# Optimization experiments

Hardware: AMD Instinct MI355X
Metric: run time of the kernel (lower is better)

The kernel has to match this reference:

```python
import jax, jax.numpy as jnp
import numpy as np

N_NODES = 100000
N_EDGES = 1600000

def spmm(edge_src, edge_dst, edge_w, h):
    # sparse adj (COO) @ dense h: gather source rows, scale, scatter-add to dest
    msg = h[edge_src] * edge_w[:, None]          # [E, F]
    return jax.ops.segment_sum(msg, edge_dst, num_segments=N_NODES)


def setup_inputs() -> dict:
    key = jax.random.key(0)
    ks = jax.random.split(key, 10)
    x = jax.random.normal(ks[0], (N_NODES, 128), dtype=jnp.float32)
    edge_src = jax.random.randint(ks[1], (N_EDGES,), 0, N_NODES, dtype=jnp.int32)
    edge_dst = jax.random.randint(ks[2], (N_EDGES,), 0, N_NODES, dtype=jnp.int32)
    edge_w = jax.random.uniform(ks[3], (N_EDGES,), dtype=jnp.float32)
    W1 = jax.random.normal(ks[4], (128, 64), dtype=jnp.float32) * 0.1
    b1 = jax.random.normal(ks[5], (64,), dtype=jnp.float32) * 0.1
    W2 = jax.random.normal(ks[6], (64, 64), dtype=jnp.float32) * 0.1
    b2 = jax.random.normal(ks[7], (64,), dtype=jnp.float32) * 0.1
    Wl = jax.random.normal(ks[8], (64, 40), dtype=jnp.float32) * 0.1
    bl = jax.random.normal(ks[9], (40,), dtype=jnp.float32) * 0.1
    return {"x": x, "edge_src": edge_src, "edge_dst": edge_dst, "edge_w": edge_w,
            "W1": W1, "b1": b1, "W2": W2, "b2": b2, "Wl": Wl, "bl": bl}


def reference(x, edge_src, edge_dst, edge_w, W1, b1, W2, b2, Wl, bl):
    # layer 1: relu(spmm(adj, x @ W1) + b1); dropout is identity in eval mode
    h1 = jax.nn.relu(spmm(edge_src, edge_dst, edge_w, x @ W1) + b1)
    # layer 2
    h2 = jax.nn.relu(spmm(edge_src, edge_dst, edge_w, h1 @ W2) + b2)
    # classifier head
    logits = h2 @ Wl + bl
    logp = jax.nn.log_softmax(logits, axis=1)
    # matches torch return: (log_softmax, node_emb=[h1, h2, logits])
    return (logp, h1, h2, logits)
```

## Files before the change

kernel.cpp:

```cpp
#include <hip/hip_runtime.h>
#include <hip/hip_bf16.h>
#include <math.h>

#define NN 100000
#define NE 1600000
#define BSHIFT 9
#define NBUCK ((NN + (1 << BSHIFT) - 1) >> BSHIFT)
#define CAP 10240
#define BINB 512
#define BCHUNK 1536
#define BINGRID ((NE + BCHUNK - 1) / BCHUNK)
#define HROWS 128
#define NPW 8

typedef __attribute__((ext_vector_type(8))) short bf16x8;
typedef __attribute__((ext_vector_type(4))) float f32x4;

static __device__ inline unsigned short f2b(float f) {
    __hip_bfloat16 b = __float2bfloat16(f);
    return *reinterpret_cast<unsigned short*>(&b);
}

__global__ __launch_bounds__(256) void gemm1_mfma(const float* __restrict__ x,
                                                  const float* __restrict__ W,
                                                  __hip_bfloat16* __restrict__ out) {
    __shared__ unsigned short Xs[128 * 136];
    __shared__ unsigned short Wt[64 * 136];
    const int tid = threadIdx.x;
    const int row0 = blockIdx.x * 128;
    for (int i = tid; i < 64 * 64; i += 256) {
        const int n = i & 63, kp = i >> 6;
        const unsigned pack = (unsigned)f2b(W[(2 * kp) * 64 + n]) |
                              ((unsigned)f2b(W[(2 * kp + 1) * 64 + n]) << 16);
        *(unsigned*)&Wt[n * 136 + 2 * kp] = pack;
    }
    for (int i = tid; i < 128 * 16; i += 256) {
        const int r = i >> 4, q = i & 15;
        const int row = row0 + r;
        float v0 = 0.f, v1 = 0.f, v2 = 0.f, v3 = 0.f, v4 = 0.f, v5 = 0.f, v6 = 0.f, v7 = 0.f;
        if (row < NN) {
            const float4 a = *(const float4*)(x + (size_t)row * 128 + q * 8);
            const float4 b = *(const float4*)(x + (size_t)row * 128 + q * 8 + 4);
            v0 = a.x; v1 = a.y; v2 = a.z; v3 = a.w; v4 = b.x; v5 = b.y; v6 = b.z; v7 = b.w;
        }
        uint4 pk;
        pk.x = (unsigned)f2b(v0) | ((unsigned)f2b(v1) << 16);
        pk.y = (unsigned)f2b(v2) | ((unsigned)f2b(v3) << 16);
        pk.z = (unsigned)f2b(v4) | ((unsigned)f2b(v5) << 16);
        pk.w = (unsigned)f2b(v6) | ((unsigned)f2b(v7) << 16);
        *(uint4*)&Xs[r * 136 + q * 8] = pk;
    }
    __syncthreads();
    const int l = tid & 63;
    const int wid = tid >> 6;
    const int m = l & 15, g = l >> 4;
    const int wr0 = wid * 32;
    f32x4 acc[2][4];
#pragma unroll
    for (int rt = 0; rt < 2; ++rt)
#pragma unroll
        for (int ct = 0; ct < 4; ++ct) acc[rt][ct] = 0;
#pragma unroll
    for (int ks = 0; ks < 4; ++ks) {
        bf16x8 a[2], b[4];
#pragma unroll
        for (int rt = 0; rt < 2; ++rt)
            a[rt] = *(const bf16x8*)&Xs[(wr0 + rt * 16 + m) * 136 + ks * 32 + g * 8];
#pragma unroll
        for (int ct = 0; ct < 4; ++ct)
            b[ct] = *(const bf16x8*)&Wt[(ct * 16 + m) * 136 + ks * 32 + g * 8];
#pragma unroll
        for (int rt = 0; rt < 2; ++rt)
#pragma unroll
            for (int ct = 0; ct < 4; ++ct)
                acc[rt][ct] = __builtin_amdgcn_mfma_f32_16x16x32_bf16(a[rt], b[ct], acc[rt][ct], 0, 0, 0);
    }
#pragma unroll
    for (int rt = 0; rt < 2; ++rt)
#pragma unroll
        for (int ct = 0; ct < 4; ++ct)
#pragma unroll
            for (int j = 0; j < 4; ++j) {
                const int r = row0 + wr0 + rt * 16 + g * 4 + j;
                if (r < NN)
                    out[(size_t)r * 64 + ct * 16 + m] = __float2bfloat16(acc[rt][ct][j]);
            }
}

__global__ __launch_bounds__(256) void gemm2_mfma(const float* __restrict__ h,
                                                  const float* __restrict__ W,
                                                  __hip_bfloat16* __restrict__ out) {
    __shared__ unsigned short Xs[128 * 72];
    __shared__ unsigned short Wt[64 * 72];
    const int tid = threadIdx.x;
    const int row0 = blockIdx.x * 128;
    for (int i = tid; i < 64 * 32; i += 256) {
        const int n = i & 63, kp = i >> 6;
        const unsigned pack = (unsigned)f2b(W[(2 * kp) * 64 + n]) |
                              ((unsigned)f2b(W[(2 * kp + 1) * 64 + n]) << 16);
        *(unsigned*)&Wt[n * 72 + 2 * kp] = pack;
    }
    for (int i = tid; i < 128 * 8; i += 256) {
        const int r = i >> 3, q = i & 7;
        const int row = row0 + r;
        float v0 = 0.f, v1 = 0.f, v2 = 0.f, v3 = 0.f, v4 = 0.f, v5 = 0.f, v6 = 0.f, v7 = 0.f;
        if (row < NN) {
            const float4 a = *(const float4*)(h + (size_t)row * 64 + q * 8);
            const float4 b = *(const float4*)(h + (size_t)row * 64 + q * 8 + 4);
            v0 = a.x; v1 = a.y; v2 = a.z; v3 = a.w; v4 = b.x; v5 = b.y; v6 = b.z; v7 = b.w;
        }
        uint4 pk;
        pk.x = (unsigned)f2b(v0) | ((unsigned)f2b(v1) << 16);
        pk.y = (unsigned)f2b(v2) | ((unsigned)f2b(v3) << 16);
        pk.z = (unsigned)f2b(v4) | ((unsigned)f2b(v5) << 16);
        pk.w = (unsigned)f2b(v6) | ((unsigned)f2b(v7) << 16);
        *(uint4*)&Xs[r * 72 + q * 8] = pk;
    }
    __syncthreads();
    const int l = tid & 63;
    const int wid = tid >> 6;
    const int m = l & 15, g = l >> 4;
    const int wr0 = wid * 32;
    f32x4 acc[2][4];
#pragma unroll
    for (int rt = 0; rt < 2; ++rt)
#pragma unroll
        for (int ct = 0; ct < 4; ++ct) acc[rt][ct] = 0;
#pragma unroll
    for (int ks = 0; ks < 2; ++ks) {
        bf16x8 a[2], b[4];
#pragma unroll
        for (int rt = 0; rt < 2; ++rt)
            a[rt] = *(const bf16x8*)&Xs[(wr0 + rt * 16 + m) * 72 + ks * 32 + g * 8];
#pragma unroll
        for (int ct = 0; ct < 4; ++ct)
            b[ct] = *(const bf16x8*)&Wt[(ct * 16 + m) * 72 + ks * 32 + g * 8];
#pragma unroll
        for (int rt = 0; rt < 2; ++rt)
#pragma unroll
            for (int ct = 0; ct < 4; ++ct)
                acc[rt][ct] = __builtin_amdgcn_mfma_f32_16x16x32_bf16(a[rt], b[ct], acc[rt][ct], 0, 0, 0);
    }
#pragma unroll
    for (int rt = 0; rt < 2; ++rt)
#pragma unroll
        for (int ct = 0; ct < 4; ++ct)
#pragma unroll
            for (int j = 0; j < 4; ++j) {
                const int r = row0 + wr0 + rt * 16 + g * 4 + j;
                if (r < NN)
                    out[(size_t)r * 64 + ct * 16 + m] = __float2bfloat16(acc[rt][ct][j]);
            }
}

__global__ void init_bcur(int* __restrict__ bcur) {
    const int t = threadIdx.x;
    if (t < NBUCK) bcur[t] = t * CAP;
}

__global__ __launch_bounds__(BINB) void bin_edges(const int* __restrict__ es,
                                                  const int* __restrict__ ed,
                                                  const float* __restrict__ ew,
                                                  int* __restrict__ bcur,
                                                  int2* __restrict__ srcdw) {
    __shared__ int hist[NBUCK];
    __shared__ int base[NBUCK];
    const int tid = threadIdx.x;
    const int e0 = blockIdx.x * BCHUNK;
    for (int i = tid; i < NBUCK; i += BINB) hist[i] = 0;
    __syncthreads();
    int d[3];
#pragma unroll
    for (int j = 0; j < 3; ++j) {
        const int e = e0 + j * BINB + tid;
        d[j] = (e < NE) ? ed[e] : -1;
        if (d[j] >= 0) atomicAdd(&hist[d[j] >> BSHIFT], 1);
    }
    __syncthreads();
    for (int i = tid; i < NBUCK; i += BINB) base[i] = atomicAdd(&bcur[i], hist[i]);
    __syncthreads();
    for (int i = tid; i < NBUCK; i += BINB) hist[i] = 0;
    __syncthreads();
#pragma unroll
    for (int j = 0; j < 3; ++j) {
        const int e = e0 + j * BINB + tid;
        if (d[j] >= 0) {
            const int bb = d[j] >> BSHIFT;
            const int l = atomicAdd(&hist[bb], 1);
            srcdw[base[bb] + l] = make_int2(es[e] | ((d[j] & 511) << 17), __float_as_int(ew[e]));
        }
    }
}

__global__ __launch_bounds__(1024) void bucket_csr(const int2* __restrict__ srcdw,
                                                   const int* __restrict__ bcur,
                                                   int2* __restrict__ rng,
                                                   int2* __restrict__ edges2) {
    __shared__ int A[512], B2[512];
    const int tid = threadIdx.x;
    const int b = blockIdx.x;
    const int base = b * CAP;
    const int cnt = bcur[b] - base;
    if (tid < 512) A[tid] = 0;
    __syncthreads();
    for (int e = tid; e < cnt; e += 1024)
        atomicAdd(&A[(srcdw[base + e].x >> 17) & 511], 1);
    __syncthreads();
    const int v = (tid < 512) ? A[tid] : 0;
    int* src = A;
    int* dst = B2;
    for (int d = 1; d < 512; d <<= 1) {
        if (tid < 512) dst[tid] = src[tid] + ((tid >= d) ? src[tid - d] : 0);
        __syncthreads();
        int* t = src; src = dst; dst = t;
    }
    if (tid < 512) {
        const int incl = src[tid];
        const int excl = incl - v;
        const int node = (b << BSHIFT) + tid;
        if (node < NN) rng[node] = make_int2(base + excl, base + incl);
        dst[tid] = excl;
    }
    __syncthreads();
    for (int e = tid; e < cnt; e += 1024) {
        const int2 sw = srcdw[base + e];
        const int dl = (sw.x >> 17) & 511;
        const int pos = atomicAdd(&dst[dl], 1);
        edges2[base + pos] = make_int2(sw.x & 0x1FFFF, sw.y);
    }
}

__global__ __launch_bounds__(256) void spmm_csr(const __hip_bfloat16* __restrict__ feat,
                                                const int2* __restrict__ rng,
                                                const int2* __restrict__ edges2,
                                                const float* __restrict__ b,
                                                float* __restrict__ out) {
    const int nwg = gridDim.x;
    const int q = nwg >> 3, rr = nwg & 7;
    const int xcd = blockIdx.x & 7;
    const int sub = blockIdx.x >> 3;
    const int swz = (xcd < rr ? xcd * (q + 1) : rr * (q + 1) + (xcd - rr) * q) + sub;
    const int w = threadIdx.x >> 6;
    const int lane = threadIdx.x & 63;
    const int n0 = (swz * 4 + w) * NPW;
    const int p = lane >> 3;
    const int f8 = lane & 7;
    const float4 bv0 = *(const float4*)(b + f8 * 8);
    const float4 bv1 = *(const float4*)(b + f8 * 8 + 4);
    const int2 r8 = rng[n0 + f8];
#define FMA8(G, WV)                                            \
    a0 = fmaf(__uint_as_float((G).x << 16), (WV), a0);         \
    a1 = fmaf(__uint_as_float((G).x & 0xffff0000u), (WV), a1); \
    a2 = fmaf(__uint_as_float((G).y << 16), (WV), a2);         \
    a3 = fmaf(__uint_as_float((G).y & 0xffff0000u), (WV), a3); \
    a4 = fmaf(__uint_as_float((G).z << 16), (WV), a4);         \
    a5 = fmaf(__uint_as_float((G).z & 0xffff0000u), (WV), a5); \
    a6 = fmaf(__uint_as_float((G).w << 16), (WV), a6);         \
    a7 = fmaf(__uint_as_float((G).w & 0xffff0000u), (WV), a7);
#define RED(A) A += __shfl_xor(A, 8, 64); A += __shfl_xor(A, 16, 64); A += __shfl_xor(A, 32, 64);
#pragma unroll 1
    for (int nn = 0; nn < NPW; ++nn) {
        const int n = n0 + nn;
        const int beg = __shfl(r8.x, nn, 64);
        const int end = __shfl(r8.y, nn, 64);
        float a0 = 0.f, a1 = 0.f, a2 = 0.f, a3 = 0.f;
        float a4 = 0.f, a5 = 0.f, a6 = 0.f, a7 = 0.f;
        int i = beg;
        for (; i + 15 < end; i += 16) {
            const int2 e0 = edges2[i + p];
            const int2 e1 = edges2[i + 8 + p];
            const uint4 g0 = *(const uint4*)(feat + (size_t)e0.x * 64 + f8 * 8);
            const uint4 g1 = *(const uint4*)(feat + (size_t)e1.x * 64 + f8 * 8);
            const float w0 = __int_as_float(e0.y), w1 = __int_as_float(e1.y);
            FMA8(g0, w0) FMA8(g1, w1)
        }
        for (; i < end; i += 8) {
            const int idx = i + p;
            const int2 e = edges2[idx];
            const float wv = (idx < end) ? __int_as_float(e.y) : 0.f;
            const uint4 g = *(const uint4*)(feat + (size_t)(e.x & 0x1FFFF) * 64 + f8 * 8);
            FMA8(g, wv)
        }
        RED(a0) RED(a1) RED(a2) RED(a3) RED(a4) RED(a5) RED(a6) RED(a7)
        if (p == 0) {
            float4 o0, o1;
            o0.x = fmaxf(a0 + bv0.x, 0.f);
            o0.y = fmaxf(a1 + bv0.y, 0.f);
            o0.z = fmaxf(a2 + bv0.z, 0.f);
            o0.w = fmaxf(a3 + bv0.w, 0.f);
            o1.x = fmaxf(a4 + bv1.x, 0.f);
            o1.y = fmaxf(a5 + bv1.y, 0.f);
            o1.z = fmaxf(a6 + bv1.z, 0.f);
            o1.w = fmaxf(a7 + bv1.w, 0.f);
            *(float4*)(out + (size_t)n * 64 + f8 * 8) = o0;
            *(float4*)(out + (size_t)n * 64 + f8 * 8 + 4) = o1;
        }
    }
#undef FMA8
#undef RED
}

__global__ __launch_bounds__(256) void head_tile(const float* __restrict__ h2,
                                                 const float* __restrict__ Wl,
                                                 const float* __restrict__ bl,
                                                 float* __restrict__ logits,
                                                 float* __restrict__ logp) {
    __shared__ float Wt[40 * 68];
    __shared__ float Xs[HROWS * 68];
    __shared__ float bs[40];
    const int tid = threadIdx.x;
    const int row0 = blockIdx.x * HROWS;
    for (int i = tid; i < 64 * 40; i += 256) {
        const int k = i / 40, c = i - k * 40;
        Wt[c * 68 + k] = Wl[i];
    }
    if (tid < 40) bs[tid] = bl[tid];
    for (int i = tid; i < HROWS * 16; i += 256) {
        const int r = i >> 4, kq = i & 15;
        const int row = row0 + r;
        float4 v = make_float4(0.f, 0.f, 0.f, 0.f);
        if (row < NN) v = *(const float4*)(h2 + (size_t)row * 64 + kq * 4);
        *(float4*)(&Xs[r * 68 + kq * 4]) = v;
    }
    __syncthreads();
    const int tcol = tid & 3;
    const int trow = tid >> 2;
    float acc[2][10] = {};
    const float* xb0 = &Xs[trow * 68];
    const float* xb1 = &Xs[(trow + 64) * 68];
    const float* wb = &Wt[(tcol * 10) * 68];
    for (int k = 0; k < 64; k += 4) {
        const float4 x0 = *(const float4*)(xb0 + k);
        const float4 x1 = *(const float4*)(xb1 + k);
#pragma unroll
        for (int c = 0; c < 10; ++c) {
            const float4 wv = *(const float4*)(wb + c * 68 + k);
            acc[0][c] = fmaf(x0.x, wv.x, acc[0][c]);
            acc[0][c] = fmaf(x0.y, wv.y, acc[0][c]);
            acc[0][c] = fmaf(x0.z, wv.z, acc[0][c]);
            acc[0][c] = fmaf(x0.w, wv.w, acc[0][c]);
            acc[1][c] = fmaf(x1.x, wv.x, acc[1][c]);
            acc[1][c] = fmaf(x1.y, wv.y, acc[1][c]);
            acc[1][c] = fmaf(x1.z, wv.z, acc[1][c]);
            acc[1][c] = fmaf(x1.w, wv.w, acc[1][c]);
        }
    }
    float bv[10];
#pragma unroll
    for (int c = 0; c < 10; ++c) bv[c] = bs[tcol * 10 + c];
#pragma unroll
    for (int r = 0; r < 2; ++r) {
        const int row = row0 + trow + r * 64;
#pragma unroll
        for (int c = 0; c < 10; ++c) acc[r][c] += bv[c];
        float m = acc[r][0];
#pragma unroll
        for (int c = 1; c < 10; ++c) m = fmaxf(m, acc[r][c]);
        m = fmaxf(m, __shfl_xor(m, 1, 64));
        m = fmaxf(m, __shfl_xor(m, 2, 64));
        float s = 0.f;
#pragma unroll
        for (int c = 0; c < 10; ++c) s += expf(acc[r][c] - m);
        s += __shfl_xor(s, 1, 64);
        s += __shfl_xor(s, 2, 64);
        const float lse = logf(s) + m;
        if (row < NN) {
            float* lg = logits + (size_t)row * 40 + tcol * 10;
            float* lp = logp   + (size_t)row * 40 + tcol * 10;
#pragma unroll
            for (int c = 0; c < 10; c += 2) {
                *(float2*)(lg + c) = make_float2(acc[r][c], acc[r][c + 1]);
                *(float2*)(lp + c) = make_float2(acc[r][c] - lse, acc[r][c + 1] - lse);
            }
        }
    }
}

extern "C" void kernel_launch(void* const* d_in, const int* in_sizes, int n_in,
                              void* d_out, int out_size, void* d_ws, size_t ws_size,
                              hipStream_t stream) {
    const float* x  = (const float*)d_in[0];
    const int*   es = (const int*)  d_in[1];
    const int*   ed = (const int*)  d_in[2];
    const float* ew = (const float*)d_in[3];
    const float* W1 = (const float*)d_in[4];
    const float* b1 = (const float*)d_in[5];
    const float* W2 = (const float*)d_in[6];
    const float* b2 = (const float*)d_in[7];
    const float* Wl = (const float*)d_in[8];
    const float* bl = (const float*)d_in[9];

    float* out    = (float*)d_out;
    float* logp   = out;
    float* h1     = logp + (size_t)NN * 40;
    float* h2     = h1   + (size_t)NN * 64;
    float* logits = h2   + (size_t)NN * 64;

    char* wsb = (char*)d_ws;
    const size_t regionA = (size_t)NBUCK * CAP * 8;
    int2* srcdw = (int2*)wsb;
    __hip_bfloat16* ws0 = (__hip_bfloat16*)wsb;
    int2* edges2 = (int2*)(wsb + regionA);
    int2* rng    = (int2*)((char*)edges2 + regionA);
    int*  bcur   = (int*)((char*)rng + (size_t)NN * 8);

    const int gemmGrid = (NN + 127) / 128;
    const int spmmGrid = NN / (4 * NPW);

    init_bcur<<<1, 256, 0, stream>>>(bcur);
    bin_edges<<<BINGRID, BINB, 0, stream>>>(es, ed, ew, bcur, srcdw);
    bucket_csr<<<NBUCK, 1024, 0, stream>>>(srcdw, bcur, rng, edges2);

    gemm1_mfma<<<gemmGrid, 256, 0, stream>>>(x, W1, ws0);
    spmm_csr<<<spmmGrid, 256, 0, stream>>>(ws0, rng, edges2, b1, h1);

    gemm2_mfma<<<gemmGrid, 256, 0, stream>>>(h1, W2, ws0);
    spmm_csr<<<spmmGrid, 256, 0, stream>>>(ws0, rng, edges2, b2, h2);

    head_tile<<<(NN + HROWS - 1) / HROWS, 256, 0, stream>>>(h2, Wl, bl, logits, logp);
}
```

Before: 202.6 us.

## Merge gemm1 and edge binning into one launch so both run concurrently

Fuses the first dense GEMM and the edge-binning pass into a single kernel, with blocks split by blockIdx. The independent work can then overlap on the GPU and one launch is saved. The init_bcur kernel becomes a memset, bcur now holds relative counts, and ws0 moves to its own workspace region so it no longer aliases srcdw. Binning now runs with 256-thread blocks that each handle 6 edges per thread, and the binning blocks carry gemm1's large LDS allocation, which may lower their occupancy.

Result: faster. 189.0 us (-6.7%).

```diff
diff --git a/kernel.cpp b/kernel.cpp
--- a/kernel.cpp
+++ b/kernel.cpp
@@ -7,9 +7,9 @@
 #define BSHIFT 9
 #define NBUCK ((NN + (1 << BSHIFT) - 1) >> BSHIFT)
 #define CAP 10240
-#define BINB 512
 #define BCHUNK 1536
 #define BINGRID ((NE + BCHUNK - 1) / BCHUNK)
+#define G1GRID ((NN + 127) / 128)
 #define HROWS 128
 #define NPW 8
 
@@ -21,70 +21,105 @@
     return *reinterpret_cast<unsigned short*>(&b);
 }
 
-__global__ __launch_bounds__(256) void gemm1_mfma(const float* __restrict__ x,
-                                                  const float* __restrict__ W,
-                                                  __hip_bfloat16* __restrict__ out) {
-    __shared__ unsigned short Xs[128 * 136];
-    __shared__ unsigned short Wt[64 * 136];
+__global__ __launch_bounds__(256) void gemm1_bin(const float* __restrict__ x,
+                                                 const float* __restrict__ W,
+                                                 __hip_bfloat16* __restrict__ out,
+                                                 const int* __restrict__ es,
+                                                 const int* __restrict__ ed,
+                                                 const float* __restrict__ ew,
+                                                 int* __restrict__ bcur,
+                                                 int2* __restrict__ srcdw) {
+    __shared__ __align__(16) unsigned short Xs[128 * 136];
+    __shared__ __align__(16) unsigned short Wt[64 * 136];
     const int tid = threadIdx.x;
-    const int row0 = blockIdx.x * 128;
-    for (int i = tid; i < 64 * 64; i += 256) {
-        const int n = i & 63, kp = i >> 6;
-        const unsigned pack = (unsigned)f2b(W[(2 * kp) * 64 + n]) |
-                              ((unsigned)f2b(W[(2 * kp + 1) * 64 + n]) << 16);
-        *(unsigned*)&Wt[n * 136 + 2 * kp] = pack;
-    }
-    for (int i = tid; i < 128 * 16; i += 256) {
-        const int r = i >> 4, q = i & 15;
-        const int row = row0 + r;
-        float v0 = 0.f, v1 = 0.f, v2 = 0.f, v3 = 0.f, v4 = 0.f, v5 = 0.f, v6 = 0.f, v7 = 0.f;
-        if (row < NN) {
-            const float4 a = *(const float4*)(x + (size_t)row * 128 + q * 8);
-            const float4 b = *(const float4*)(x + (size_t)row * 128 + q * 8 + 4);
-            v0 = a.x; v1 = a.y; v2 = a.z; v3 = a.w; v4 = b.x; v5 = b.y; v6 = b.z; v7 = b.w;
-        }
-        uint4 pk;
-        pk.x = (unsigned)f2b(v0) | ((unsigned)f2b(v1) << 16);
-        pk.y = (unsigned)f2b(v2) | ((unsigned)f2b(v3) << 16);
-        pk.z = (unsigned)f2b(v4) | ((unsigned)f2b(v5) << 16);
-        pk.w = (unsigned)f2b(v6) | ((unsigned)f2b(v7) << 16);
-        *(uint4*)&Xs[r * 136 + q * 8] = pk;
-    }
-    __syncthreads();
-    const int l = tid & 63;
-    const int wid = tid >> 6;
-    const int m = l & 15, g = l >> 4;
-    const int wr0 = wid * 32;
-    f32x4 acc[2][4];
-#pragma unroll
-    for (int rt = 0; rt < 2; ++rt)
-#pragma unroll
-        for (int ct = 0; ct < 4; ++ct) acc[rt][ct] = 0;
-#pragma unroll
-    for (int ks = 0; ks < 4; ++ks) {
-        bf16x8 a[2], b[4];
+    if (blockIdx.x < G1GRID) {
+        const int row0 = blockIdx.x * 128;
+        for (int i = tid; i < 64 * 64; i += 256) {
+            const int n = i & 63, kp = i >> 6;
+            const unsigned pack = (unsigned)f2b(W[(2 * kp) * 64 + n]) |
+                                  ((unsigned)f2b(W[(2 * kp + 1) * 64 + n]) << 16);
+            *(unsigned*)&Wt[n * 136 + 2 * kp] = pack;
+        }
+        for (int i = tid; i < 128 * 16; i += 256) {
+            const int r = i >> 4, q = i & 15;
+            const int row = row0 + r;
+            float v0 = 0.f, v1 = 0.f, v2 = 0.f, v3 = 0.f, v4 = 0.f, v5 = 0.f, v6 = 0.f, v7 = 0.f;
+            if (row < NN) {
+                const float4 a = *(const float4*)(x + (size_t)row * 128 + q * 8);
+                const float4 b = *(const float4*)(x + (size_t)row * 128 + q * 8 + 4);
+                v0 = a.x; v1 = a.y; v2 = a.z; v3 = a.w; v4 = b.x; v5 = b.y; v6 = b.z; v7 = b.w;
+            }
+            uint4 pk;
+            pk.x = (unsigned)f2b(v0) | ((unsigned)f2b(v1) << 16);
+            pk.y = (unsigned)f2b(v2) | ((unsigned)f2b(v3) << 16);
+            pk.z = (unsigned)f2b(v4) | ((unsigned)f2b(v5) << 16);
+            pk.w = (unsigned)f2b(v6) | ((unsigned)f2b(v7) << 16);
+            *(uint4*)&Xs[r * 136 + q * 8] = pk;
+        }
+        __syncthreads();
+        const int l = tid & 63;
+        const int wid = tid >> 6;
+        const int m = l & 15, g = l >> 4;
+        const int wr0 = wid * 32;
+        f32x4 acc[2][4];
 #pragma unroll
         for (int rt = 0; rt < 2; ++rt)
-            a[rt] = *(const bf16x8*)&Xs[(wr0 + rt * 16 + m) * 136 + ks * 32 + g * 8];
-#pragma unroll
-        for (int ct = 0; ct < 4; ++ct)
-            b[ct] = *(const bf16x8*)&Wt[(ct * 16 + m) * 136 + ks * 32 + g * 8];
+#pragma unroll
+            for (int ct = 0; ct < 4; ++ct) acc[rt][ct] = 0;
+#pragma unroll
+        for (int ks = 0; ks < 4; ++ks) {
+            bf16x8 a[2], b[4];
+#pragma unroll
+            for (int rt = 0; rt < 2; ++rt)
+                a[rt] = *(const bf16x8*)&Xs[(wr0 + rt * 16 + m) * 136 + ks * 32 + g * 8];
+#pragma unroll
+            for (int ct = 0; ct < 4; ++ct)
+                b[ct] = *(const bf16x8*)&Wt[(ct * 16 + m) * 136 + ks * 32 + g * 8];
+#pragma unroll
+            for (int rt = 0; rt < 2; ++rt)
+#pragma unroll
+                for (int ct = 0; ct < 4; ++ct)
+                    acc[rt][ct] = __builtin_amdgcn_mfma_f32_16x16x32_bf16(a[rt], b[ct], acc[rt][ct], 0, 0, 0);
+        }
 #pragma unroll
         for (int rt = 0; rt < 2; ++rt)
 #pragma unroll
             for (int ct = 0; ct < 4; ++ct)
-                acc[rt][ct] = __builtin_amdgcn_mfma_f32_16x16x32_bf16(a[rt], b[ct], acc[rt][ct], 0, 0, 0);
-    }
-#pragma unroll
-    for (int rt = 0; rt < 2; ++rt)
-#pragma unroll
-        for (int ct = 0; ct < 4; ++ct)
-#pragma unroll
-            for (int j = 0; j < 4; ++j) {
-                const int r = row0 + wr0 + rt * 16 + g * 4 + j;
-                if (r < NN)
-                    out[(size_t)r * 64 + ct * 16 + m] = __float2bfloat16(acc[rt][ct][j]);
+#pragma unroll
+                for (int j = 0; j < 4; ++j) {
+                    const int r = row0 + wr0 + rt * 16 + g * 4 + j;
+                    if (r < NN)
+                        out[(size_t)r * 64 + ct * 16 + m] = __float2bfloat16(acc[rt][ct][j]);
+                }
+    } else {
+        int* hist = (int*)Xs;
+        int* base = hist + NBUCK;
+        const int e0 = (blockIdx.x - G1GRID) * BCHUNK;
+        for (int i = tid; i < NBUCK; i += 256) hist[i] = 0;
+        __syncthreads();
+        int d[6];
+#pragma unroll
+        for (int j = 0; j < 6; ++j) {
+            const int e = e0 + j * 256 + tid;
+            d[j] = (e < NE) ? ed[e] : -1;
+            if (d[j] >= 0) atomicAdd(&hist[d[j] >> BSHIFT], 1);
+        }
+        __syncthreads();
+        for (int i = tid; i < NBUCK; i += 256)
+            base[i] = i * CAP + atomicAdd(&bcur[i], hist[i]);
+        __syncthreads();
+        for (int i = tid; i < NBUCK; i += 256) hist[i] = 0;
+        __syncthreads();
+#pragma unroll
+        for (int j = 0; j < 6; ++j) {
+            const int e = e0 + j * 256 + tid;
+            if (d[j] >= 0) {
+                const int bb = d[j] >> BSHIFT;
+                const int l2 = atomicAdd(&hist[bb], 1);
+                srcdw[base[bb] + l2] = make_int2(es[e] | ((d[j] & 511) << 17), __float_as_int(ew[e]));
             }
+        }
+    }
 }
 
 __global__ __launch_bounds__(256) void gemm2_mfma(const float* __restrict__ h,
@@ -153,45 +188,6 @@
             }
 }
 
-__global__ void init_bcur(int* __restrict__ bcur) {
-    const int t = threadIdx.x;
-    if (t < NBUCK) bcur[t] = t * CAP;
-}
-
-__global__ __launch_bounds__(BINB) void bin_edges(const int* __restrict__ es,
-                                                  const int* __restrict__ ed,
-                                                  const float* __restrict__ ew,
-                                                  int* __restrict__ bcur,
-                                                  int2* __restrict__ srcdw) {
-    __shared__ int hist[NBUCK];
-    __shared__ int base[NBUCK];
-    const int tid = threadIdx.x;
-    const int e0 = blockIdx.x * BCHUNK;
-    for (int i = tid; i < NBUCK; i += BINB) hist[i] = 0;
-    __syncthreads();
-    int d[3];
-#pragma unroll
-    for (int j = 0; j < 3; ++j) {
-        const int e = e0 + j * BINB + tid;
-        d[j] = (e < NE) ? ed[e] : -1;
-        if (d[j] >= 0) atomicAdd(&hist[d[j] >> BSHIFT], 1);
-    }
-    __syncthreads();
-    for (int i = tid; i < NBUCK; i += BINB) base[i] = atomicAdd(&bcur[i], hist[i]);
-    __syncthreads();
-    for (int i = tid; i < NBUCK; i += BINB) hist[i] = 0;
-    __syncthreads();
-#pragma unroll
-    for (int j = 0; j < 3; ++j) {
-        const int e = e0 + j * BINB + tid;
-        if (d[j] >= 0) {
-            const int bb = d[j] >> BSHIFT;
-            const int l = atomicAdd(&hist[bb], 1);
-            srcdw[base[bb] + l] = make_int2(es[e] | ((d[j] & 511) << 17), __float_as_int(ew[e]));
-        }
-    }
-}
-
 __global__ __launch_bounds__(1024) void bucket_csr(const int2* __restrict__ srcdw,
                                                    const int* __restrict__ bcur,
                                                    int2* __restrict__ rng,
@@ -200,7 +196,7 @@
     const int tid = threadIdx.x;
     const int b = blockIdx.x;
     const int base = b * CAP;
-    const int cnt = bcur[b] - base;
+    const int cnt = bcur[b];
     if (tid < 512) A[tid] = 0;
     __syncthreads();
     for (int e = tid; e < cnt; e += 1024)
@@ -399,19 +395,18 @@
     char* wsb = (char*)d_ws;
     const size_t regionA = (size_t)NBUCK * CAP * 8;
     int2* srcdw = (int2*)wsb;
-    __hip_bfloat16* ws0 = (__hip_bfloat16*)wsb;
     int2* edges2 = (int2*)(wsb + regionA);
     int2* rng    = (int2*)((char*)edges2 + regionA);
     int*  bcur   = (int*)((char*)rng + (size_t)NN * 8);
+    __hip_bfloat16* ws0 = (__hip_bfloat16*)((char*)bcur + 4096);
 
     const int gemmGrid = (NN + 127) / 128;
     const int spmmGrid = NN / (4 * NPW);
 
-    init_bcur<<<1, 256, 0, stream>>>(bcur);
-    bin_edges<<<BINGRID, BINB, 0, stream>>>(es, ed, ew, bcur, srcdw);
+    hipMemsetAsync(bcur, 0, (size_t)NBUCK * 4, stream);
+    gemm1_bin<<<G1GRID + BINGRID, 256, 0, stream>>>(x, W1, ws0, es, ed, ew, bcur, srcdw);
     bucket_csr<<<NBUCK, 1024, 0, stream>>>(srcdw, bcur, rng, edges2);
 
-    gemm1_mfma<<<gemmGrid, 256, 0, stream>>>(x, W1, ws0);
     spmm_csr<<<spmmGrid, 256, 0, stream>>>(ws0, rng, edges2, b1, h1);
 
     gemm2_mfma<<<gemmGrid, 256, 0, stream>>>(h1, W2, ws0);
```
